# Kernel tuning notes

Measured on AMD Instinct MI355X. Metric: run time of the kernel, lower is better.

Reference implementation:

```python
import jax, jax.numpy as jnp
import numpy as np

FS = 512
SEQ_LEN = 16384
BATCH = 128
TAPS = 513  # common kernel length; per-band kernels zero-padded at the tail
N_BANDS = 20


def _design_kernels():
    """Windowed-sinc (fir1/firwin-style, hamming) bandpass kernels, tensorpac-like."""
    pha = [(f, f + 2.0) for f in np.arange(2.0, 22.0, 2.0)]    # 10 phase bands
    amp = [(f, f + 10.0) for f in np.arange(30.0, 130.0, 10.0)]  # 10 amp bands
    cycles = [3] * 10 + [6] * 10
    bands = pha + amp
    K = np.zeros((N_BANDS, TAPS), np.float32)
    for i, ((lo, hi), c) in enumerate(zip(bands, cycles)):
        order = min(int(c * FS / lo), TAPS - 1)  # fir_order ~ cycle * fs / low_hz
        taps = order + 1
        n = np.arange(taps) - (taps - 1) / 2.0
        f1, f2 = lo / FS, hi / FS
        h = 2.0 * f2 * np.sinc(2.0 * f2 * n) - 2.0 * f1 * np.sinc(2.0 * f1 * n)
        h *= np.hamming(taps)
        K[i, :taps] = h.astype(np.float32)
    return jnp.asarray(K)


def setup_inputs() -> dict:
    key = jax.random.key(0)
    x = jax.random.normal(key, (BATCH, 1, SEQ_LEN), dtype=jnp.float32)
    return {"x": x, "kernels": _design_kernels(), "padlen": TAPS - 1}


def _filtfilt_bands(x2d, kernels, P):
    """scipy.signal.filtfilt(b, 1.0, x, padlen=P) for all bands at once.
    x2d: (B, L); kernels: (nb, T) FIR taps. Odd-extension padding + lfilter_zi
    initial conditions (== constant extension of the first sample by T-1)."""
    B, L = x2d.shape
    nb, T = kernels.shape
    # odd extension: left_j = 2*x[0] - x[P-j], right_j = 2*x[-1] - x[-2-j]
    left = 2.0 * x2d[:, :1] - x2d[:, 1:P + 1][:, ::-1]
    right = 2.0 * x2d[:, -1:] - x2d[:, -P - 1:-1][:, ::-1]
    ext = jnp.concatenate([left, x2d, right], axis=1)  # (B, L + 2P)
    krev = kernels[:, ::-1][:, None, :]  # (nb, 1, T); correlation with b[::-1] == causal conv with b

    def causal_conv(sig, groups):
        # sig: (B, C, Ls); constant left-extension by T-1 (lfilter zi*x0 semantics)
        pad = jnp.repeat(sig[..., :1], T - 1, axis=-1)
        s = jnp.concatenate([pad, sig], axis=-1)
        return jax.lax.conv_general_dilated(
            s, krev, (1,), 'VALID',
            dimension_numbers=('NCW', 'OIW', 'NCW'),
            feature_group_count=groups)

    y = causal_conv(ext[:, None, :], 1)        # forward pass -> (B, nb, L+2P)
    y2 = causal_conv(y[:, :, ::-1], nb)        # backward pass (grouped, per-band)
    return y2[:, :, ::-1][:, :, P:P + L]       # un-reverse and trim padding


def reference(x, kernels, padlen):
    # x: (B, 1, L) -> (B, 1, n_bands, L)
    out = _filtfilt_bands(x[:, 0, :], kernels, padlen)
    return out[:, None, :, :]
```

## Files before the change

### kernel.cpp

```cpp
#include <hip/hip_runtime.h>

#define LSEQ   16384
#define NB     20
#define NBATCH 128
#define TAPS   513
#define CT     (2*TAPS - 1)
#define MAXSTEP 72

#define TT     2048
#define SPANE  3088
#define STRIDE 3096
#define EXTEND 16896
#define GMAX   17407

#define HDR_OFF  0
#define MMX_OFF  256
#define CS_OFF   4096
#define CSTRIDE  1040
#define ATAB_OFF 98304

typedef short  v8s  __attribute__((ext_vector_type(8)));
typedef __bf16 v8bf __attribute__((ext_vector_type(8)));
typedef float  v16f __attribute__((ext_vector_type(16)));

__device__ __forceinline__ unsigned short f2bf(float f) {
    union { float f; unsigned u; } v; v.f = f;
    return (unsigned short)((v.u + 0x7fffu + ((v.u >> 16) & 1u)) >> 16);
}

__device__ __forceinline__ v16f vzero() {
    v16f z;
    #pragma unroll
    for (int i = 0; i < 16; ++i) z[i] = 0.f;
    return z;
}

__global__ __launch_bounds__(512) void autoc_kernel(
    const float* __restrict__ Kg, float* __restrict__ Cs, int2* __restrict__ mmx)
{
    __shared__ __align__(16) float kk[TAPS];
    __shared__ float ps[512];
    __shared__ int smin, smax;
    const int band = blockIdx.x, y = blockIdx.y;
    const int tid = threadIdx.x;
    const int rel = tid & 127, q = tid >> 7;
    const int d = 128 * y + rel;

    for (int i = tid; i < TAPS; i += 512) kk[i] = Kg[band * TAPS + i];
    if (tid == 0) { smin = CT; smax = 0; }
    __syncthreads();

    float s = 0.f;
    if (d < CT) {
        int al = d - 512; if (al < 0) al = -al;
        const int n = TAPS - al;
        const int nq = (((n + 3) >> 2) + 3) & ~3;
        int i0 = q * nq, i1 = i0 + nq; if (i1 > n) i1 = n;
        float s0 = 0.f, s1 = 0.f, s2 = 0.f, s3 = 0.f;
        int i = i0;
        for (; i + 3 < i1; i += 4) {
            s0 = fmaf(kk[i],     kk[i + al],     s0);
            s1 = fmaf(kk[i + 1], kk[i + 1 + al], s1);
            s2 = fmaf(kk[i + 2], kk[i + 2 + al], s2);
            s3 = fmaf(kk[i + 3], kk[i + 3 + al], s3);
        }
        for (; i < i1; ++i) s0 = fmaf(kk[i], kk[i + al], s0);
        s = (s0 + s1) + (s2 + s3);
    }
    ps[tid] = s;
    __syncthreads();
    if (q == 0 && d < CT) {
        float tot = (ps[rel] + ps[rel + 128]) + (ps[rel + 256] + ps[rel + 384]);
        Cs[band * CSTRIDE + d] = tot;
        if (tot != 0.f) { atomicMin(&smin, d); atomicMax(&smax, d); }
    }
    __syncthreads();
    if (tid == 0) { int2 r; r.x = smin; r.y = smax; mmx[band * 9 + y] = r; }
}

__global__ __launch_bounds__(1024) void table_kernel(
    const float* __restrict__ Cs, const int2* __restrict__ mmx,
    int2* __restrict__ hdr, short* __restrict__ atab)
{
    __shared__ int sk0, sN;
    const int band = blockIdx.x, tid = threadIdx.x;
    if (tid == 0) {
        int mn = CT, mx = 0;
        for (int j = 0; j < 9; ++j) {
            int2 r = mmx[band * 9 + j];
            if (r.x < mn) mn = r.x;
            if (r.y > mx) mx = r.y;
        }
        int k0 = mn & ~15;
        int k1 = ((mx + 31) >> 4) << 4;
        int N  = (k1 - k0) / 16 + 1;
        int2 h; h.x = k0; h.y = N;
        hdr[band] = h;
        sk0 = k0; sN = N;
    }
    __syncthreads();
    const int k0 = sk0, N = sN;
    int nf = N + 3; if (nf > MAXSTEP) nf = MAXSTEP;
    const float* cb = Cs + band * CSTRIDE;
    for (int idx = tid; idx < nf * 64; idx += 1024) {
        int s = idx >> 6, lane = idx & 63;
        int m = lane & 31, kh = lane >> 5;
        int base = k0 + 16 * s + 8 * kh - m;
        v8s r;
        #pragma unroll
        for (int j = 0; j < 8; ++j) {
            int ci = base + j;
            float v = (ci >= 0 && ci < CT) ? cb[ci] : 0.f;
            r[j] = (short)f2bf(v);
        }
        *(v8s*)(atab + ((size_t)(band * MAXSTEP + s) * 64 + lane) * 8) = r;
    }
}

__global__ __launch_bounds__(256, 3) void filt_main(
    const float* __restrict__ x, const short* __restrict__ atab,
    const int2* __restrict__ hdr, float* __restrict__ out)
{
    __shared__ __align__(16) unsigned short extl[8 * STRIDE];
    const int tid = threadIdx.x;
    const int tile = blockIdx.x, grp = blockIdx.y, bg = blockIdx.z;
    const int T0 = tile * TT;

    const bool edge = (T0 < 512) || (T0 + SPANE > EXTEND);
    for (int b = 0; b < 8; ++b) {
        const float* xb = x + (size_t)(bg * 8 + b) * LSEQ;
        float x0 = 0.f, xN = 0.f;
        if (edge) { x0 = xb[0]; xN = xb[LSEQ - 1]; }
        for (int e4 = tid; e4 < SPANE / 4; e4 += 256) {
            const int e = 4 * e4;
            const int g0 = T0 + e;
            float v0, v1, v2, v3;
            if (g0 >= 512 && g0 + 4 <= EXTEND) {
                float4 xv = *(const float4*)(xb + (g0 - 512));
                v0 = xv.x; v1 = xv.y; v2 = xv.z; v3 = xv.w;
            } else {
                float vv[4];
                #pragma unroll
                for (int t = 0; t < 4; ++t) {
                    int g = g0 + t; if (g > GMAX) g = GMAX;
                    vv[t] = (g < 512)    ? 2.f * x0 - xb[512 - g]
                          : (g < EXTEND) ? xb[g - 512]
                          :                2.f * xN - xb[2 * LSEQ + 512 - 2 - g];
                }
                v0 = vv[0]; v1 = vv[1]; v2 = vv[2]; v3 = vv[3];
            }
            ushort4 qv = make_ushort4(f2bf(v0), f2bf(v1), f2bf(v2), f2bf(v3));
            *(ushort4*)&extl[b * STRIDE + e] = qv;
        }
    }
    __syncthreads();

    const int lane = tid & 63;
    const int w    = tid >> 6;
    const int n    = lane & 31, kh = lane >> 5;
    const int brow = n & 7,  tb = n >> 3;
    const unsigned short* bpb = extl + brow * STRIDE + 512 * w + 32 * tb + 8 * kh;

    const int g_start[6] = {0, 4, 8, 11, 15, 20};
    const int g_list[20] = {0,19,18,17, 1,16,15,14, 2,3,13, 4,5,6,12, 7,8,9,10,11};

    for (int bi = g_start[grp]; bi < g_start[grp + 1]; ++bi) {
        const int band = g_list[bi];
        const int2 hh = hdr[band];
        const int k0 = hh.x, N = hh.y;
        const unsigned short* bp = bpb + k0;
        const short* ap = atab + (size_t)(band * MAXSTEP) * 512 + lane * 8;

        v16f ac0 = vzero(), ac1 = vzero(), ac2 = vzero(), ac3 = vzero();
        v8bf A0 = __builtin_bit_cast(v8bf, *(const v8s*)ap);
        v8bf A1 = __builtin_bit_cast(v8bf, *(const v8s*)(ap + 512));
        v8bf A2 = __builtin_bit_cast(v8bf, *(const v8s*)(ap + 1024));
        v8bf B0 = *(const v8bf*)(bp);
        v8bf B1 = *(const v8bf*)(bp + 128);
        v8bf B2 = *(const v8bf*)(bp + 256);
        v8bf B3 = *(const v8bf*)(bp + 384);

        #pragma unroll 2
        for (int s = 0; s < N; ++s) {
            v8bf An  = __builtin_bit_cast(v8bf, *(const v8s*)(ap + (size_t)(s + 3) * 512));
            const unsigned short* bn = bp + 16 * (s + 1);
            v8bf Bn0 = *(const v8bf*)(bn);
            v8bf Bn1 = *(const v8bf*)(bn + 128);
            v8bf Bn2 = *(const v8bf*)(bn + 256);
            v8bf Bn3 = *(const v8bf*)(bn + 384);
            __builtin_amdgcn_s_setprio(1);
            ac0 = __builtin_amdgcn_mfma_f32_32x32x16_bf16(A0, B0, ac0, 0, 0, 0);
            ac1 = __builtin_amdgcn_mfma_f32_32x32x16_bf16(A0, B1, ac1, 0, 0, 0);
            ac2 = __builtin_amdgcn_mfma_f32_32x32x16_bf16(A0, B2, ac2, 0, 0, 0);
            ac3 = __builtin_amdgcn_mfma_f32_32x32x16_bf16(A0, B3, ac3, 0, 0, 0);
            __builtin_amdgcn_s_setprio(0);
            A0 = A1; A1 = A2; A2 = An;
            B0 = Bn0; B1 = Bn1; B2 = Bn2; B3 = Bn3;
        }

        float* ob = out + ((size_t)(bg * 8 + brow) * NB + band) * LSEQ
                        + T0 + 512 * w + 32 * tb + 4 * kh;
        #pragma unroll
        for (int q = 0; q < 4; ++q) {
            *(float4*)(ob +       8 * q) = make_float4(ac0[4*q], ac0[4*q+1], ac0[4*q+2], ac0[4*q+3]);
            *(float4*)(ob + 128 + 8 * q) = make_float4(ac1[4*q], ac1[4*q+1], ac1[4*q+2], ac1[4*q+3]);
            *(float4*)(ob + 256 + 8 * q) = make_float4(ac2[4*q], ac2[4*q+1], ac2[4*q+2], ac2[4*q+3]);
            *(float4*)(ob + 384 + 8 * q) = make_float4(ac3[4*q], ac3[4*q+1], ac3[4*q+2], ac3[4*q+3]);
        }
    }
}

extern "C" void kernel_launch(void* const* d_in, const int* in_sizes, int n_in,
                              void* d_out, int out_size, void* d_ws, size_t ws_size,
                              hipStream_t stream) {
    const float* x  = (const float*)d_in[0];
    const float* Kg = (const float*)d_in[1];
    float* out = (float*)d_out;

    char* wsb = (char*)d_ws;
    int2*  hdr  = (int2*)(wsb + HDR_OFF);
    int2*  mmx  = (int2*)(wsb + MMX_OFF);
    float* Cs   = (float*)(wsb + CS_OFF);
    short* atab = (short*)(wsb + ATAB_OFF);

    autoc_kernel<<<dim3(NB, 9), dim3(512), 0, stream>>>(Kg, Cs, mmx);
    table_kernel<<<dim3(NB), dim3(1024), 0, stream>>>(Cs, mmx, hdr, atab);
    filt_main<<<dim3(LSEQ / TT, 5, NBATCH / 8), dim3(256), 0, stream>>>(x, atab, hdr, out);
}
```

Baseline: 223.1 us.

## Use nontemporal output stores, vectorize autocorrelation LDS reads, move min/max to table kernel

Output stores in the main MFMA filter kernel become nontemporal, so the large streamed output does not pollute the cache. The autocorrelation kernel keeps four shifted copies of the taps in LDS, so the lagged reads can use aligned float4 loads. The nonzero-range min/max search moves from the autocorrelation kernel into the table kernel, which also stages the coefficients in LDS. The setup kernels are tiny, so the store hint on the output-bound main kernel is what matters; the risk is little change or slight write-path differences.

After: 353.7 us. +58.5%, slower.

```diff
diff --git a/kernel.cpp b/kernel.cpp
--- a/kernel.cpp
+++ b/kernel.cpp
@@ -14,7 +14,6 @@
 #define GMAX   17407
 
 #define HDR_OFF  0
-#define MMX_OFF  256
 #define CS_OFF   4096
 #define CSTRIDE  1040
 #define ATAB_OFF 98304
@@ -22,6 +21,7 @@
 typedef short  v8s  __attribute__((ext_vector_type(8)));
 typedef __bf16 v8bf __attribute__((ext_vector_type(8)));
 typedef float  v16f __attribute__((ext_vector_type(16)));
+typedef float  v4f  __attribute__((ext_vector_type(4)));
 
 __device__ __forceinline__ unsigned short f2bf(float f) {
     union { float f; unsigned u; } v; v.f = f;
@@ -35,36 +35,53 @@
     return z;
 }
 
+__device__ __forceinline__ void nt_store4(float* p, float a, float b, float c, float d) {
+    v4f v; v[0] = a; v[1] = b; v[2] = c; v[3] = d;
+    __builtin_nontemporal_store(v, (v4f*)p);
+}
+
 __global__ __launch_bounds__(512) void autoc_kernel(
-    const float* __restrict__ Kg, float* __restrict__ Cs, int2* __restrict__ mmx)
+    const float* __restrict__ Kg, float* __restrict__ Cs)
 {
-    __shared__ __align__(16) float kk[TAPS];
+    __shared__ __align__(16) float kk4[4][520];
     __shared__ float ps[512];
-    __shared__ int smin, smax;
     const int band = blockIdx.x, y = blockIdx.y;
     const int tid = threadIdx.x;
     const int rel = tid & 127, q = tid >> 7;
     const int d = 128 * y + rel;
 
-    for (int i = tid; i < TAPS; i += 512) kk[i] = Kg[band * TAPS + i];
-    if (tid == 0) { smin = CT; smax = 0; }
+    for (int j = tid; j < TAPS; j += 512) {
+        float v = Kg[band * TAPS + j];
+        kk4[0][j] = v;
+        if (j >= 1) kk4[1][j - 1] = v;
+        if (j >= 2) kk4[2][j - 2] = v;
+        if (j >= 3) kk4[3][j - 3] = v;
+    }
+    if (tid < 40) {
+        int c = tid / 10, t = tid % 10;
+        int j = 510 + t;
+        if (j >= TAPS - c && j < 520) kk4[c][j] = 0.f;
+    }
     __syncthreads();
 
     float s = 0.f;
     if (d < CT) {
         int al = d - 512; if (al < 0) al = -al;
-        const int n = TAPS - al;
+        const int n  = TAPS - al;
+        const int c  = al & 3, sh4 = (al >> 2) << 2;
         const int nq = (((n + 3) >> 2) + 3) & ~3;
         int i0 = q * nq, i1 = i0 + nq; if (i1 > n) i1 = n;
         float s0 = 0.f, s1 = 0.f, s2 = 0.f, s3 = 0.f;
         int i = i0;
         for (; i + 3 < i1; i += 4) {
-            s0 = fmaf(kk[i],     kk[i + al],     s0);
-            s1 = fmaf(kk[i + 1], kk[i + 1 + al], s1);
-            s2 = fmaf(kk[i + 2], kk[i + 2 + al], s2);
-            s3 = fmaf(kk[i + 3], kk[i + 3 + al], s3);
-        }
-        for (; i < i1; ++i) s0 = fmaf(kk[i], kk[i + al], s0);
+            float4 a = *(const float4*)&kk4[0][i];
+            float4 b = *(const float4*)&kk4[c][i + sh4];
+            s0 = fmaf(a.x, b.x, s0);
+            s1 = fmaf(a.y, b.y, s1);
+            s2 = fmaf(a.z, b.z, s2);
+            s3 = fmaf(a.w, b.w, s3);
+        }
+        for (; i < i1; ++i) s0 = fmaf(kk4[0][i], kk4[c][i + sh4], s0);
         s = (s0 + s1) + (s2 + s3);
     }
     ps[tid] = s;
@@ -72,36 +89,41 @@
     if (q == 0 && d < CT) {
         float tot = (ps[rel] + ps[rel + 128]) + (ps[rel + 256] + ps[rel + 384]);
         Cs[band * CSTRIDE + d] = tot;
-        if (tot != 0.f) { atomicMin(&smin, d); atomicMax(&smax, d); }
-    }
-    __syncthreads();
-    if (tid == 0) { int2 r; r.x = smin; r.y = smax; mmx[band * 9 + y] = r; }
+    }
 }
 
 __global__ __launch_bounds__(1024) void table_kernel(
-    const float* __restrict__ Cs, const int2* __restrict__ mmx,
-    int2* __restrict__ hdr, short* __restrict__ atab)
+    const float* __restrict__ Cs, int2* __restrict__ hdr, short* __restrict__ atab)
 {
-    __shared__ int sk0, sN;
+    __shared__ float csh[CT];
+    __shared__ int smin, smax, sk0, sN;
     const int band = blockIdx.x, tid = threadIdx.x;
+    if (tid == 0) { smin = CT; smax = 0; }
+    __syncthreads();
+
+    const float* cb = Cs + band * CSTRIDE;
+    int lmin = CT, lmax = 0;
+    for (int j = tid; j < CT; j += 1024) {
+        float v = cb[j];
+        csh[j] = v;
+        if (v != 0.f) { if (j < lmin) lmin = j; if (j > lmax) lmax = j; }
+    }
+    if (lmin < CT) atomicMin(&smin, lmin);
+    if (lmax > 0)  atomicMax(&smax, lmax);
+    __syncthreads();
+
     if (tid == 0) {
-        int mn = CT, mx = 0;
-        for (int j = 0; j < 9; ++j) {
-            int2 r = mmx[band * 9 + j];
-            if (r.x < mn) mn = r.x;
-            if (r.y > mx) mx = r.y;
-        }
-        int k0 = mn & ~15;
-        int k1 = ((mx + 31) >> 4) << 4;
+        int k0 = smin & ~15;
+        int k1 = ((smax + 31) >> 4) << 4;
         int N  = (k1 - k0) / 16 + 1;
         int2 h; h.x = k0; h.y = N;
         hdr[band] = h;
         sk0 = k0; sN = N;
     }
     __syncthreads();
+
     const int k0 = sk0, N = sN;
     int nf = N + 3; if (nf > MAXSTEP) nf = MAXSTEP;
-    const float* cb = Cs + band * CSTRIDE;
     for (int idx = tid; idx < nf * 64; idx += 1024) {
         int s = idx >> 6, lane = idx & 63;
         int m = lane & 31, kh = lane >> 5;
@@ -110,7 +132,7 @@
         #pragma unroll
         for (int j = 0; j < 8; ++j) {
             int ci = base + j;
-            float v = (ci >= 0 && ci < CT) ? cb[ci] : 0.f;
+            float v = (ci >= 0 && ci < CT) ? csh[ci] : 0.f;
             r[j] = (short)f2bf(v);
         }
         *(v8s*)(atab + ((size_t)(band * MAXSTEP + s) * 64 + lane) * 8) = r;
@@ -202,10 +224,10 @@
                         + T0 + 512 * w + 32 * tb + 4 * kh;
         #pragma unroll
         for (int q = 0; q < 4; ++q) {
-            *(float4*)(ob +       8 * q) = make_float4(ac0[4*q], ac0[4*q+1], ac0[4*q+2], ac0[4*q+3]);
-            *(float4*)(ob + 128 + 8 * q) = make_float4(ac1[4*q], ac1[4*q+1], ac1[4*q+2], ac1[4*q+3]);
-            *(float4*)(ob + 256 + 8 * q) = make_float4(ac2[4*q], ac2[4*q+1], ac2[4*q+2], ac2[4*q+3]);
-            *(float4*)(ob + 384 + 8 * q) = make_float4(ac3[4*q], ac3[4*q+1], ac3[4*q+2], ac3[4*q+3]);
+            nt_store4(ob +       8 * q, ac0[4*q], ac0[4*q+1], ac0[4*q+2], ac0[4*q+3]);
+            nt_store4(ob + 128 + 8 * q, ac1[4*q], ac1[4*q+1], ac1[4*q+2], ac1[4*q+3]);
+            nt_store4(ob + 256 + 8 * q, ac2[4*q], ac2[4*q+1], ac2[4*q+2], ac2[4*q+3]);
+            nt_store4(ob + 384 + 8 * q, ac3[4*q], ac3[4*q+1], ac3[4*q+2], ac3[4*q+3]);
         }
     }
 }
@@ -219,11 +241,10 @@
 
     char* wsb = (char*)d_ws;
     int2*  hdr  = (int2*)(wsb + HDR_OFF);
-    int2*  mmx  = (int2*)(wsb + MMX_OFF);
     float* Cs   = (float*)(wsb + CS_OFF);
     short* atab = (short*)(wsb + ATAB_OFF);
 
-    autoc_kernel<<<dim3(NB, 9), dim3(512), 0, stream>>>(Kg, Cs, mmx);
-    table_kernel<<<dim3(NB), dim3(1024), 0, stream>>>(Cs, mmx, hdr, atab);
+    autoc_kernel<<<dim3(NB, 9), dim3(512), 0, stream>>>(Kg, Cs);
+    table_kernel<<<dim3(NB), dim3(1024), 0, stream>>>(Cs, hdr, atab);
     filt_main<<<dim3(LSEQ / TT, 5, NBATCH / 8), dim3(256), 0, stream>>>(x, atab, hdr, out);
 }
```
